# Optimization experiments

Measured on AMD Instinct MI355X. Metric: run time of the kernel, lower is better.

## Reference

```python
import jax, jax.numpy as jnp
import numpy as np

N, C_IN, C_OUT, H, W = 16, 256, 256, 32, 32
K = 9  # 3x3 kernel


def setup_inputs() -> dict:
    key = jax.random.key(0)
    k1, k2, k3 = jax.random.split(key, 3)
    x = jax.random.normal(k1, (N, C_IN, H, W), dtype=jnp.float32)
    # offsets as produced upstream from anchors: (N, H*W, 18)
    offset = jax.random.normal(k2, (N, H * W, 2 * K), dtype=jnp.float32)
    # DeformConv weight (no bias), kaiming-ish scale
    weight = jax.random.normal(k3, (C_OUT, C_IN, 3, 3), dtype=jnp.float32) * 0.02
    return {"x": x, "offset": offset, "weight": weight}


def _deform_conv3x3(x, offset_nchw, weight):
    """DeformConv v1, kernel 3x3, stride 1, padding 1, dilation 1,
    groups=1, deformable_groups=1, zero padding outside borders."""
    n, c, h, w = x.shape
    o = weight.shape[0]
    # offset channel layout: (dy_k, dx_k) pairs for k = 0..8
    off = offset_nchw.reshape(n, K, 2, h, w)
    dy = off[:, :, 0]  # (N,K,H,W)
    dx = off[:, :, 1]
    ky = (jnp.arange(K) // 3 - 1).astype(x.dtype)  # kernel row offsets -1,0,1
    kx = (jnp.arange(K) % 3 - 1).astype(x.dtype)
    base_y = jnp.arange(h, dtype=x.dtype)[None, None, :, None]
    base_x = jnp.arange(w, dtype=x.dtype)[None, None, None, :]
    py = base_y + ky[None, :, None, None] + dy  # (N,K,H,W) sample rows
    px = base_x + kx[None, :, None, None] + dx  # (N,K,H,W) sample cols

    y0 = jnp.floor(py)
    x0 = jnp.floor(px)
    ly = py - y0  # fractional parts
    lx = px - x0

    x_flat = x.reshape(n, c, h * w)

    def corner(yi, xi, wgt):
        valid = (yi >= 0) & (yi <= h - 1) & (xi >= 0) & (xi <= w - 1)
        yc = jnp.clip(yi, 0, h - 1).astype(jnp.int32)
        xc = jnp.clip(xi, 0, w - 1).astype(jnp.int32)
        idx = (yc * w + xc).reshape(n, K * h * w)
        g = jax.vmap(lambda xf, i: xf[:, i])(x_flat, idx)  # (N,C,K*H*W)
        wv = (wgt * valid.astype(x.dtype)).reshape(n, 1, K * h * w)
        return g * wv

    val = (corner(y0, x0, (1 - ly) * (1 - lx))
           + corner(y0, x0 + 1, (1 - ly) * lx)
           + corner(y0 + 1, x0, ly * (1 - lx))
           + corner(y0 + 1, x0 + 1, ly * lx))
    val = val.reshape(n, c, K, h, w)  # sampled im2col columns
    return jnp.einsum('nckhw,ock->nohw', val, weight.reshape(o, c, K))


def reference(x, offset, weight):
    n, _, h, w = x.shape
    assert h * w == offset.shape[1]
    # AdaptiveConv.forward: (N, HW, 18) -> (N, 18, H, W)
    offset_nchw = jnp.transpose(offset, (0, 2, 1)).reshape(n, 2 * K, h, w)
    return _deform_conv3x3(x, offset_nchw, weight)
```

## Files before the change

### kernel.cpp

```cpp
#include <hip/hip_runtime.h>
#include <hip/hip_bf16.h>

#define NB   16
#define CIN  256
#define COUT 256
#define HH   32
#define WW   32
#define HW   1024
#define KK   9
#define CK   2304

typedef __bf16 bf16x8 __attribute__((ext_vector_type(8)));
typedef float  f32x4  __attribute__((ext_vector_type(4)));

__device__ __forceinline__ unsigned short f2bf(float f) {
    unsigned int u = __float_as_uint(f);
    u += 0x7FFFu + ((u >> 16) & 1u);
    return (unsigned short)(u >> 16);
}
__device__ __forceinline__ float bfhi(unsigned int u) {
    return __uint_as_float(u & 0xFFFF0000u);
}
__device__ __forceinline__ float bflo(unsigned int u) {
    return __uint_as_float(u << 16);
}

__global__ __launch_bounds__(256) void wconv_kernel(const float* __restrict__ w,
                                                    unsigned short* __restrict__ wbf) {
    __shared__ float ls[CK];
    const int o = blockIdx.x;
    const float* wo = w + (size_t)o * CK;
#pragma unroll
    for (int i = threadIdx.x; i < CK; i += 256) ls[i] = wo[i];
    __syncthreads();
    unsigned short* dst = wbf + (size_t)o * CK;
#pragma unroll
    for (int i = threadIdx.x; i < CK; i += 256) {
        int k = i >> 8, c = i & 255;
        dst[i] = f2bf(ls[c * KK + k]);
    }
}

__global__ __launch_bounds__(256) void xt_kernel(const float* __restrict__ x,
                                                 unsigned short* __restrict__ xtb) {
    __shared__ float ls[64][65];
    const int c0  = blockIdx.x * 64;
    const int hw0 = blockIdx.y * 64;
    const int n   = blockIdx.z;
    const int t   = threadIdx.x;
    {
        int c = t >> 2, q = t & 3;
        const float4* base = (const float4*)(x + ((size_t)(n * CIN + c0 + c)) * HW + hw0 + q * 16);
#pragma unroll
        for (int j = 0; j < 4; ++j) {
            float4 v = base[j];
            ls[c][q * 16 + j * 4 + 0] = v.x;
            ls[c][q * 16 + j * 4 + 1] = v.y;
            ls[c][q * 16 + j * 4 + 2] = v.z;
            ls[c][q * 16 + j * 4 + 3] = v.w;
        }
    }
    __syncthreads();
    {
        int hw = t >> 2, seg = (t & 3) * 16;
        unsigned int dw[8];
#pragma unroll
        for (int j = 0; j < 8; ++j) {
            float f0 = ls[seg + 2 * j][hw];
            float f1 = ls[seg + 2 * j + 1][hw];
            dw[j] = (unsigned)f2bf(f0) | ((unsigned)f2bf(f1) << 16);
        }
        uint4* dst = (uint4*)(xtb + ((size_t)(n * HW + hw0 + hw)) * CIN + c0 + seg);
        dst[0] = *(uint4*)&dw[0];
        dst[1] = *(uint4*)&dw[4];
    }
}

__global__ __launch_bounds__(512, 2) void fused_kernel(const unsigned short* __restrict__ wbf,
                                                       const unsigned short* __restrict__ xtb,
                                                       const float* __restrict__ off,
                                                       float* __restrict__ out) {
    __shared__ unsigned short Bs[2][64 * 64];

    const int tid  = threadIdx.x;
    const int wv   = tid >> 6;
    const int lane = tid & 63;
    const int quad = lane >> 4;
    const int l15  = lane & 15;

    const int hwl = tid >> 3;
    const int seg = tid & 7;

    const int id  = blockIdx.x;
    const int n   = ((id & 7) << 1) | ((id >> 3) & 1);
    const int hw0 = (id >> 4) * 64;

    const int hw = hw0 + hwl;
    const int h  = hw >> 5, w = hw & 31;

    const uint4*  xb4  = (const uint4*)(xtb + (size_t)n * HW * CIN);
    const float2* offp = (const float2*)(off + ((size_t)n * HW + hw) * (2 * KK));
    const unsigned short* Abase = wbf + (size_t)(wv * 32 + l15) * CK + quad * 8;

    f32x4 acc[2][4] = {};

    auto setup = [&](int tap, float wg[4], int ix[4]) {
        float2 o = offp[tap];
        float py = (float)(h + tap / 3 - 1) + o.x;
        float px = (float)(w + tap % 3 - 1) + o.y;
        float y0f = floorf(py), x0f = floorf(px);
        float ly = py - y0f, lx = px - x0f;
        int y0 = (int)y0f, x0 = (int)x0f;
#pragma unroll
        for (int c2 = 0; c2 < 4; ++c2) {
            int yy = y0 + (c2 >> 1);
            int xx = x0 + (c2 & 1);
            float wy = (c2 >> 1) ? ly : 1.0f - ly;
            float wx = (c2 & 1) ? lx : 1.0f - lx;
            bool v = (yy >= 0) && (yy < HH) && (xx >= 0) && (xx < WW);
            wg[c2] = v ? wy * wx : 0.0f;
            int yc = yy < 0 ? 0 : (yy > HH - 1 ? HH - 1 : yy);
            int xc = xx < 0 ? 0 : (xx > WW - 1 ? WW - 1 : xx);
            ix[c2] = yc * WW + xc;
        }
    };

    auto loadc = [&](uint4 cr[4], const int ix[4], int s) {
        int sub = s & 3;
#pragma unroll
        for (int c2 = 0; c2 < 4; ++c2)
            cr[c2] = xb4[(size_t)ix[c2] * 32 + sub * 8 + seg];
    };

    auto loada = [&](bf16x8 af[2][2], int s) {
        const unsigned short* p = Abase + s * 64;
#pragma unroll
        for (int mi = 0; mi < 2; ++mi)
#pragma unroll
            for (int hh = 0; hh < 2; ++hh)
                af[mi][hh] = *(const bf16x8*)(p + (size_t)mi * 16 * CK + hh * 32);
    };

    auto buildB = [&](int nb, const uint4 cr[4], const float wg[4]) {
        unsigned u0[4], u1[4], u2[4], u3[4];
        *(uint4*)u0 = cr[0]; *(uint4*)u1 = cr[1];
        *(uint4*)u2 = cr[2]; *(uint4*)u3 = cr[3];
        unsigned dw[4];
#pragma unroll
        for (int d = 0; d < 4; ++d) {
            float2 lv;
            lv.x = wg[0] * bflo(u0[d]) + wg[1] * bflo(u1[d])
                 + wg[2] * bflo(u2[d]) + wg[3] * bflo(u3[d]);
            lv.y = wg[0] * bfhi(u0[d]) + wg[1] * bfhi(u1[d])
                 + wg[2] * bfhi(u2[d]) + wg[3] * bfhi(u3[d]);
            __hip_bfloat162 bb = __float22bfloat162_rn(lv);
            dw[d] = *(unsigned*)&bb;
        }
        *(uint4*)&Bs[nb][hwl * 64 + (seg ^ (hwl & 7)) * 8] = *(uint4*)dw;
    };

    auto mfma_step = [&](int pb, const bf16x8 af[2][2]) {
        bf16x8 bfr[4][2];
#pragma unroll
        for (int ni = 0; ni < 4; ++ni)
#pragma unroll
            for (int hh = 0; hh < 2; ++hh) {
                int row = ni * 16 + l15;
                int ch  = (hh * 4 + quad) ^ (row & 7);
                bfr[ni][hh] = *(const bf16x8*)&Bs[pb][row * 64 + ch * 8];
            }
#pragma unroll
        for (int mi = 0; mi < 2; ++mi)
#pragma unroll
            for (int ni = 0; ni < 4; ++ni) {
                acc[mi][ni] = __builtin_amdgcn_mfma_f32_16x16x32_bf16(af[mi][0], bfr[ni][0], acc[mi][ni], 0, 0, 0);
                acc[mi][ni] = __builtin_amdgcn_mfma_f32_16x16x32_bf16(af[mi][1], bfr[ni][1], acc[mi][ni], 0, 0, 0);
            }
    };

    float wgc[4], wgn[4];
    int   ixc[4], ixn[4];
    uint4 crE[4], crO[4];
    bf16x8 afE[2][2], afO[2][2];

    setup(0, wgc, ixc);
    loadc(crE, ixc, 0);
    loadc(crO, ixc, 1);
    loada(afE, 0);
    buildB(0, crE, wgc);
    __syncthreads();

    for (int tap = 0; tap < 9; ++tap) {
        const int b = tap * 4;
        buildB(1, crO, wgc);
        loadc(crE, ixc, b + 2);
        loada(afO, b + 1);
        mfma_step(0, afE);
        __syncthreads();
        buildB(0, crE, wgc);
        loadc(crO, ixc, b + 3);
        loada(afE, b + 2);
        mfma_step(1, afO);
        __syncthreads();
        buildB(1, crO, wgc);
        if (tap < 8) { setup(tap + 1, wgn, ixn); loadc(crE, ixn, b + 4); }
        loada(afO, b + 3);
        mfma_step(0, afE);
        __syncthreads();
        if (tap < 8) {
            buildB(0, crE, wgn);
            loadc(crO, ixn, b + 5);
            loada(afE, b + 4);
#pragma unroll
            for (int c2 = 0; c2 < 4; ++c2) { wgc[c2] = wgn[c2]; ixc[c2] = ixn[c2]; }
            mfma_step(1, afO);
            __syncthreads();
        } else {
            mfma_step(1, afO);
        }
    }

    float* opnt = out + (size_t)n * COUT * HW + hw0;
#pragma unroll
    for (int mi = 0; mi < 2; ++mi)
#pragma unroll
        for (int ni = 0; ni < 4; ++ni) {
            int col = ni * 16 + l15;
#pragma unroll
            for (int rr = 0; rr < 4; ++rr) {
                int row = wv * 32 + mi * 16 + quad * 4 + rr;
                opnt[(size_t)row * HW + col] = acc[mi][ni][rr];
            }
        }
}

extern "C" void kernel_launch(void* const* d_in, const int* in_sizes, int n_in,
                              void* d_out, int out_size, void* d_ws, size_t ws_size,
                              hipStream_t stream) {
    const float* x   = (const float*)d_in[0];
    const float* off = (const float*)d_in[1];
    const float* wt  = (const float*)d_in[2];
    float* out = (float*)d_out;

    unsigned short* wbf = (unsigned short*)d_ws;
    unsigned short* xtb = (unsigned short*)((char*)d_ws + 1179648);

    wconv_kernel<<<256, 256, 0, stream>>>(wt, wbf);
    xt_kernel<<<dim3(4, 16, 16), 256, 0, stream>>>(x, xtb);
    fused_kernel<<<256, 512, 0, stream>>>(wbf, xtb, off, out);
}
```

Measured before the change: 127.1 us.

## Stage a whole tap's 256-channel B tile per barrier instead of 64-channel slices

Each pipeline stage now covers a full 3x3 tap: the B buffer grows from 64 to 256 channels per pixel, every thread issues all 16 bilinear corner gathers for the next tap in one batch, and the MFMA work for four channel slices runs between barriers. This cuts barriers from four per tap to one and overlaps the gathers for the next tap with the second half of the MFMAs. The cost is more LDS (64 KB double-buffered) and many more registers for the gathered data and A fragments. With launch_bounds(512,2) that may force spills or reduce occupancy.

```diff
diff --git a/kernel.cpp b/kernel.cpp
--- a/kernel.cpp
+++ b/kernel.cpp
@@ -80,7 +80,7 @@
                                                        const unsigned short* __restrict__ xtb,
                                                        const float* __restrict__ off,
                                                        float* __restrict__ out) {
-    __shared__ unsigned short Bs[2][64 * 64];
+    __shared__ unsigned short Bs[2][64 * 256];
 
     const int tid  = threadIdx.x;
     const int wv   = tid >> 6;
@@ -104,8 +104,7 @@
 
     f32x4 acc[2][4] = {};
 
-    auto setup = [&](int tap, float wg[4], int ix[4]) {
-        float2 o = offp[tap];
+    auto setup = [&](float2 o, int tap, float wg[4], int ix[4]) {
         float py = (float)(h + tap / 3 - 1) + o.x;
         float px = (float)(w + tap % 3 - 1) + o.y;
         float y0f = floorf(py), x0f = floorf(px);
@@ -125,23 +124,15 @@
         }
     };
 
-    auto loadc = [&](uint4 cr[4], const int ix[4], int s) {
-        int sub = s & 3;
-#pragma unroll
-        for (int c2 = 0; c2 < 4; ++c2)
-            cr[c2] = xb4[(size_t)ix[c2] * 32 + sub * 8 + seg];
-    };
-
-    auto loada = [&](bf16x8 af[2][2], int s) {
-        const unsigned short* p = Abase + s * 64;
-#pragma unroll
-        for (int mi = 0; mi < 2; ++mi)
-#pragma unroll
-            for (int hh = 0; hh < 2; ++hh)
-                af[mi][hh] = *(const bf16x8*)(p + (size_t)mi * 16 * CK + hh * 32);
-    };
-
-    auto buildB = [&](int nb, const uint4 cr[4], const float wg[4]) {
+    auto loadc = [&](uint4 cr[16], const int ix[4]) {
+#pragma unroll
+        for (int s = 0; s < 4; ++s)
+#pragma unroll
+            for (int c2 = 0; c2 < 4; ++c2)
+                cr[s * 4 + c2] = xb4[(size_t)ix[c2] * 32 + s * 8 + seg];
+    };
+
+    auto buildB = [&](int nb, int s, const uint4* cr, const float wg[4]) {
         unsigned u0[4], u1[4], u2[4], u3[4];
         *(uint4*)u0 = cr[0]; *(uint4*)u1 = cr[1];
         *(uint4*)u2 = cr[2]; *(uint4*)u3 = cr[3];
@@ -156,68 +147,73 @@
             __hip_bfloat162 bb = __float22bfloat162_rn(lv);
             dw[d] = *(unsigned*)&bb;
         }
-        *(uint4*)&Bs[nb][hwl * 64 + (seg ^ (hwl & 7)) * 8] = *(uint4*)dw;
-    };
-
-    auto mfma_step = [&](int pb, const bf16x8 af[2][2]) {
+        *(uint4*)&Bs[nb][hwl * 256 + (s * 8 + (seg ^ (hwl & 7))) * 8] = *(uint4*)dw;
+    };
+
+    auto mfma_sub = [&](int pb, int s, const bf16x8 af2[2][2]) {
         bf16x8 bfr[4][2];
 #pragma unroll
         for (int ni = 0; ni < 4; ++ni)
 #pragma unroll
             for (int hh = 0; hh < 2; ++hh) {
                 int row = ni * 16 + l15;
-                int ch  = (hh * 4 + quad) ^ (row & 7);
-                bfr[ni][hh] = *(const bf16x8*)&Bs[pb][row * 64 + ch * 8];
+                int ch  = s * 8 + ((hh * 4 + quad) ^ (row & 7));
+                bfr[ni][hh] = *(const bf16x8*)&Bs[pb][row * 256 + ch * 8];
             }
 #pragma unroll
         for (int mi = 0; mi < 2; ++mi)
 #pragma unroll
             for (int ni = 0; ni < 4; ++ni) {
-                acc[mi][ni] = __builtin_amdgcn_mfma_f32_16x16x32_bf16(af[mi][0], bfr[ni][0], acc[mi][ni], 0, 0, 0);
-                acc[mi][ni] = __builtin_amdgcn_mfma_f32_16x16x32_bf16(af[mi][1], bfr[ni][1], acc[mi][ni], 0, 0, 0);
+                acc[mi][ni] = __builtin_amdgcn_mfma_f32_16x16x32_bf16(af2[mi][0], bfr[ni][0], acc[mi][ni], 0, 0, 0);
+                acc[mi][ni] = __builtin_amdgcn_mfma_f32_16x16x32_bf16(af2[mi][1], bfr[ni][1], acc[mi][ni], 0, 0, 0);
             }
     };
 
-    float wgc[4], wgn[4];
-    int   ixc[4], ixn[4];
-    uint4 crE[4], crO[4];
-    bf16x8 afE[2][2], afO[2][2];
-
-    setup(0, wgc, ixc);
-    loadc(crE, ixc, 0);
-    loadc(crO, ixc, 1);
-    loada(afE, 0);
-    buildB(0, crE, wgc);
+    {
+        float wg0[4]; int ix0[4]; uint4 cr0[16];
+        float2 o0 = offp[0];
+        setup(o0, 0, wg0, ix0);
+        loadc(cr0, ix0);
+#pragma unroll
+        for (int s = 0; s < 4; ++s) buildB(0, s, &cr0[s * 4], wg0);
+    }
     __syncthreads();
 
     for (int tap = 0; tap < 9; ++tap) {
-        const int b = tap * 4;
-        buildB(1, crO, wgc);
-        loadc(crE, ixc, b + 2);
-        loada(afO, b + 1);
-        mfma_step(0, afE);
+        const int pb = tap & 1;
+
+        bf16x8 af[4][2][2];
+        {
+            const unsigned short* pA = Abase + tap * 256;
+#pragma unroll
+            for (int s = 0; s < 4; ++s)
+#pragma unroll
+                for (int mi = 0; mi < 2; ++mi)
+#pragma unroll
+                    for (int hh = 0; hh < 2; ++hh)
+                        af[s][mi][hh] = *(const bf16x8*)(pA + (size_t)mi * 16 * CK + s * 64 + hh * 32);
+        }
+
+        float2 onxt;
+        if (tap < 8) onxt = offp[tap + 1];
+
+        mfma_sub(pb, 0, af[0]);
+        mfma_sub(pb, 1, af[1]);
+
+        float wgn[4]; int ixn[4]; uint4 crs[16];
+        if (tap < 8) {
+            setup(onxt, tap + 1, wgn, ixn);
+            loadc(crs, ixn);
+        }
+
+        mfma_sub(pb, 2, af[2]);
+        mfma_sub(pb, 3, af[3]);
+
+        if (tap < 8) {
+#pragma unroll
+            for (int s = 0; s < 4; ++s) buildB(pb ^ 1, s, &crs[s * 4], wgn);
+        }
         __syncthreads();
-        buildB(0, crE, wgc);
-        loadc(crO, ixc, b + 3);
-        loada(afE, b + 2);
-        mfma_step(1, afO);
-        __syncthreads();
-        buildB(1, crO, wgc);
-        if (tap < 8) { setup(tap + 1, wgn, ixn); loadc(crE, ixn, b + 4); }
-        loada(afO, b + 3);
-        mfma_step(0, afE);
-        __syncthreads();
-        if (tap < 8) {
-            buildB(0, crE, wgn);
-            loadc(crO, ixn, b + 5);
-            loada(afE, b + 4);
-#pragma unroll
-            for (int c2 = 0; c2 < 4; ++c2) { wgc[c2] = wgn[c2]; ixc[c2] = ixn[c2]; }
-            mfma_step(1, afO);
-            __syncthreads();
-        } else {
-            mfma_step(1, afO);
-        }
     }
 
     float* opnt = out + (size_t)n * COUT * HW + hw0;
```

Result: no change. 128.9 us (+1.4%).

## Split fused deform-conv tiles into smaller blocks covering half the output channels

Applied to the files above, without the earlier changes.

Changes the fused kernel tiling from 64 pixels × 256 output channels per 512-thread block to 32 pixels × 128 output channels per 256-thread block, launching 1024 blocks instead of 256. This aims to fill more compute units and raise occupancy, since the old grid was roughly one block per unit. In exchange, each pixel's bilinear gather and B-tile construction is repeated for both output-channel halves, doubling gather traffic per MFMA. The pipeline is restructured into a uniform two-stage loop over 36 k-steps.

```diff
diff --git a/kernel.cpp b/kernel.cpp
--- a/kernel.cpp
+++ b/kernel.cpp
@@ -76,11 +76,11 @@
     }
 }
 
-__global__ __launch_bounds__(512, 2) void fused_kernel(const unsigned short* __restrict__ wbf,
+__global__ __launch_bounds__(256, 3) void fused_kernel(const unsigned short* __restrict__ wbf,
                                                        const unsigned short* __restrict__ xtb,
                                                        const float* __restrict__ off,
                                                        float* __restrict__ out) {
-    __shared__ unsigned short Bs[2][64 * 64];
+    __shared__ unsigned short Bs[2][32 * 64];
 
     const int tid  = threadIdx.x;
     const int wv   = tid >> 6;
@@ -93,18 +93,22 @@
 
     const int id  = blockIdx.x;
     const int n   = ((id & 7) << 1) | ((id >> 3) & 1);
-    const int hw0 = (id >> 4) * 64;
+    const int hw0 = ((id >> 4) & 31) * 32;
+    const int mh  = id >> 9;
 
     const int hw = hw0 + hwl;
     const int h  = hw >> 5, w = hw & 31;
 
-    const uint4*  xb4  = (const uint4*)(xtb + (size_t)n * HW * CIN);
-    const float2* offp = (const float2*)(off + ((size_t)n * HW + hw) * (2 * KK));
-    const unsigned short* Abase = wbf + (size_t)(wv * 32 + l15) * CK + quad * 8;
-
-    f32x4 acc[2][4] = {};
-
-    auto setup = [&](int tap, float wg[4], int ix[4]) {
+    const unsigned short* xb   = xtb + (size_t)n * HW * CIN;
+    const float2*         offp = (const float2*)(off + ((size_t)n * HW + hw) * (2 * KK));
+    const unsigned short* Abase = wbf + (size_t)(mh * 128 + wv * 32 + l15) * CK + quad * 8;
+
+    f32x4 acc[2][2] = {};
+
+    float wgI[4];
+    int   ixI[4];
+
+    auto setup = [&](int tap) {
         float2 o = offp[tap];
         float py = (float)(h + tap / 3 - 1) + o.x;
         float px = (float)(w + tap % 3 - 1) + o.y;
@@ -118,30 +122,23 @@
             float wy = (c2 >> 1) ? ly : 1.0f - ly;
             float wx = (c2 & 1) ? lx : 1.0f - lx;
             bool v = (yy >= 0) && (yy < HH) && (xx >= 0) && (xx < WW);
-            wg[c2] = v ? wy * wx : 0.0f;
+            wgI[c2] = v ? wy * wx : 0.0f;
             int yc = yy < 0 ? 0 : (yy > HH - 1 ? HH - 1 : yy);
             int xc = xx < 0 ? 0 : (xx > WW - 1 ? WW - 1 : xx);
-            ix[c2] = yc * WW + xc;
-        }
-    };
-
-    auto loadc = [&](uint4 cr[4], const int ix[4], int s) {
-        int sub = s & 3;
+            ixI[c2] = yc * WW + xc;
+        }
+    };
+
+    auto issue = [&](int t, uint4 cr[4], float wgs[4]) {
+        int sub = t & 3;
 #pragma unroll
         for (int c2 = 0; c2 < 4; ++c2)
-            cr[c2] = xb4[(size_t)ix[c2] * 32 + sub * 8 + seg];
-    };
-
-    auto loada = [&](bf16x8 af[2][2], int s) {
-        const unsigned short* p = Abase + s * 64;
-#pragma unroll
-        for (int mi = 0; mi < 2; ++mi)
-#pragma unroll
-            for (int hh = 0; hh < 2; ++hh)
-                af[mi][hh] = *(const bf16x8*)(p + (size_t)mi * 16 * CK + hh * 32);
-    };
-
-    auto buildB = [&](int nb, const uint4 cr[4], const float wg[4]) {
+            cr[c2] = *(const uint4*)(xb + (size_t)ixI[c2] * CIN + sub * 64 + seg * 8);
+#pragma unroll
+        for (int c2 = 0; c2 < 4; ++c2) wgs[c2] = wgI[c2];
+    };
+
+    auto build = [&](int nb, const uint4 cr[4], const float wgs[4]) {
         unsigned u0[4], u1[4], u2[4], u3[4];
         *(uint4*)u0 = cr[0]; *(uint4*)u1 = cr[1];
         *(uint4*)u2 = cr[2]; *(uint4*)u3 = cr[3];
@@ -149,20 +146,29 @@
 #pragma unroll
         for (int d = 0; d < 4; ++d) {
             float2 lv;
-            lv.x = wg[0] * bflo(u0[d]) + wg[1] * bflo(u1[d])
-                 + wg[2] * bflo(u2[d]) + wg[3] * bflo(u3[d]);
-            lv.y = wg[0] * bfhi(u0[d]) + wg[1] * bfhi(u1[d])
-                 + wg[2] * bfhi(u2[d]) + wg[3] * bfhi(u3[d]);
+            lv.x = wgs[0] * bflo(u0[d]) + wgs[1] * bflo(u1[d])
+                 + wgs[2] * bflo(u2[d]) + wgs[3] * bflo(u3[d]);
+            lv.y = wgs[0] * bfhi(u0[d]) + wgs[1] * bfhi(u1[d])
+                 + wgs[2] * bfhi(u2[d]) + wgs[3] * bfhi(u3[d]);
             __hip_bfloat162 bb = __float22bfloat162_rn(lv);
             dw[d] = *(unsigned*)&bb;
         }
         *(uint4*)&Bs[nb][hwl * 64 + (seg ^ (hwl & 7)) * 8] = *(uint4*)dw;
     };
 
+    auto loadA = [&](bf16x8 af[2][2], int s) {
+        const unsigned short* p = Abase + s * 64;
+#pragma unroll
+        for (int mi = 0; mi < 2; ++mi)
+#pragma unroll
+            for (int hh = 0; hh < 2; ++hh)
+                af[mi][hh] = *(const bf16x8*)(p + (size_t)mi * 16 * CK + hh * 32);
+    };
+
     auto mfma_step = [&](int pb, const bf16x8 af[2][2]) {
-        bf16x8 bfr[4][2];
-#pragma unroll
-        for (int ni = 0; ni < 4; ++ni)
+        bf16x8 bfr[2][2];
+#pragma unroll
+        for (int ni = 0; ni < 2; ++ni)
 #pragma unroll
             for (int hh = 0; hh < 2; ++hh) {
                 int row = ni * 16 + l15;
@@ -172,63 +178,52 @@
 #pragma unroll
         for (int mi = 0; mi < 2; ++mi)
 #pragma unroll
-            for (int ni = 0; ni < 4; ++ni) {
+            for (int ni = 0; ni < 2; ++ni) {
                 acc[mi][ni] = __builtin_amdgcn_mfma_f32_16x16x32_bf16(af[mi][0], bfr[ni][0], acc[mi][ni], 0, 0, 0);
                 acc[mi][ni] = __builtin_amdgcn_mfma_f32_16x16x32_bf16(af[mi][1], bfr[ni][1], acc[mi][ni], 0, 0, 0);
             }
     };
 
-    float wgc[4], wgn[4];
-    int   ixc[4], ixn[4];
-    uint4 crE[4], crO[4];
-    bf16x8 afE[2][2], afO[2][2];
-
-    setup(0, wgc, ixc);
-    loadc(crE, ixc, 0);
-    loadc(crO, ixc, 1);
-    loada(afE, 0);
-    buildB(0, crE, wgc);
+    float wgA[4], wgB[4];
+    uint4 crA[4], crB[4];
+    bf16x8 afA[2][2], afB[2][2];
+
+    setup(0);
+    issue(0, crA, wgA);
+    loadA(afA, 0);
+    build(0, crA, wgA);
+    issue(1, crB, wgB);
     __syncthreads();
 
-    for (int tap = 0; tap < 9; ++tap) {
-        const int b = tap * 4;
-        buildB(1, crO, wgc);
-        loadc(crE, ixc, b + 2);
-        loada(afO, b + 1);
-        mfma_step(0, afE);
+    for (int sp = 0; sp < 18; ++sp) {
+        const int s = sp * 2;
+        if (s < 35) build(1, crB, wgB);
+        if (s + 2 < 36) {
+            if (((s + 2) & 3) == 0) setup((s + 2) >> 2);
+            issue(s + 2, crA, wgA);
+        }
+        if (s < 35) loadA(afB, s + 1);
+        mfma_step(0, afA);
         __syncthreads();
-        buildB(0, crE, wgc);
-        loadc(crO, ixc, b + 3);
-        loada(afE, b + 2);
-        mfma_step(1, afO);
+        if (s + 1 < 35) build(0, crA, wgA);
+        if (s + 3 < 36) {
+            if (((s + 3) & 3) == 0) setup((s + 3) >> 2);
+            issue(s + 3, crB, wgB);
+        }
+        if (s + 1 < 35) loadA(afA, s + 2);
+        mfma_step(1, afB);
         __syncthreads();
-        buildB(1, crO, wgc);
-        if (tap < 8) { setup(tap + 1, wgn, ixn); loadc(crE, ixn, b + 4); }
-        loada(afO, b + 3);
-        mfma_step(0, afE);
-        __syncthreads();
-        if (tap < 8) {
-            buildB(0, crE, wgn);
-            loadc(crO, ixn, b + 5);
-            loada(afE, b + 4);
-#pragma unroll
-            for (int c2 = 0; c2 < 4; ++c2) { wgc[c2] = wgn[c2]; ixc[c2] = ixn[c2]; }
-            mfma_step(1, afO);
-            __syncthreads();
-        } else {
-            mfma_step(1, afO);
-        }
     }
 
     float* opnt = out + (size_t)n * COUT * HW + hw0;
 #pragma unroll
     for (int mi = 0; mi < 2; ++mi)
 #pragma unroll
-        for (int ni = 0; ni < 4; ++ni) {
+        for (int ni = 0; ni < 2; ++ni) {
             int col = ni * 16 + l15;
 #pragma unroll
             for (int rr = 0; rr < 4; ++rr) {
-                int row = wv * 32 + mi * 16 + quad * 4 + rr;
+                int row = mh * 128 + wv * 32 + mi * 16 + quad * 4 + rr;
                 opnt[(size_t)row * HW + col] = acc[mi][ni][rr];
             }
         }
@@ -247,5 +242,5 @@
 
     wconv_kernel<<<256, 256, 0, stream>>>(wt, wbf);
     xt_kernel<<<dim3(4, 16, 16), 256, 0, stream>>>(x, xtb);
-    fused_kernel<<<256, 512, 0, stream>>>(wbf, xtb, off, out);
-}
+    fused_kernel<<<1024, 256, 0, stream>>>(wbf, xtb, off, out);
+}
```

After: 163.3 us. 28.5% more time.
